# Optimization experiments

Hardware: AMD Instinct MI355X
Metric: run time of the kernel (lower is better)

## Reference

```python
import jax, jax.numpy as jnp
import numpy as np

EPS = 1e-5

def _layernorm(x, gamma, beta):
    # normalize over last (channel) axis, per point
    mu = jnp.mean(x, axis=-1, keepdims=True)
    var = jnp.mean(jnp.square(x - mu), axis=-1, keepdims=True)
    return (x - mu) * jax.lax.rsqrt(var + EPS) * gamma + beta

def setup_inputs() -> dict:
    key = jax.random.key(0)
    ks = jax.random.split(key, 12)
    B, N, C, F = 32, 4096, 3, 1024
    points = jax.random.normal(ks[0], (B, N, C), dtype=jnp.float32)
    mask = jax.random.randint(ks[1], (B, 1, N), 0, 2, dtype=jnp.int32)
    s = 0.05
    return {
        "points": points,
        "mask": mask,
        "w1": jax.random.normal(ks[2], (128, C), dtype=jnp.float32) * s,      # conv1 (no bias)
        "g1": jnp.ones((128,), jnp.float32),                                   # norm1 gamma
        "be1": jnp.zeros((128,), jnp.float32),                                 # norm1 beta
        "w2": jax.random.normal(ks[3], (256, 128), dtype=jnp.float32) * s,     # conv2
        "b2": jax.random.normal(ks[4], (256,), dtype=jnp.float32) * s,
        "w3": jax.random.normal(ks[5], (512, 512), dtype=jnp.float32) * s,     # conv3 (no bias)
        "g2": jnp.ones((512,), jnp.float32),                                   # norm2 gamma
        "be2": jnp.zeros((512,), jnp.float32),                                 # norm2 beta
        "w4": jax.random.normal(ks[6], (F, 512), dtype=jnp.float32) * s,       # conv4
        "b4": jax.random.normal(ks[7], (F,), dtype=jnp.float32) * s,
    }

def reference(points, mask, w1, g1, be1, w2, b2, w3, g2, be2, w4, b4):
    # points: [B, N, C]; mask: [B, 1, N]
    vis = (mask[:, 0, :] != 0).astype(points.dtype)[..., None]  # [B, N, 1]
    # conv1 (1x1, no bias) as point-wise matmul
    h0 = jnp.einsum('bnc,kc->bnk', points, w1)                  # [B, N, 128]
    # masked LayerNorm: LN is per-point over channels, so compute densely and zero invisible points
    h1 = _layernorm(h0, g1, be1) * vis
    h2 = jax.nn.relu(h1)
    h3 = jnp.einsum('bnk,ok->bno', h2, w2) + b2                 # [B, N, 256]
    gmax = jnp.max(h3, axis=1, keepdims=True)                   # [B, 1, 256]
    dist = jnp.concatenate([jnp.broadcast_to(gmax, h3.shape), h3], axis=-1)  # [B, N, 512]
    h4 = jnp.einsum('bno,po->bnp', dist, w3)                    # [B, N, 512]
    h5 = _layernorm(h4, g2, be2) * vis
    h6 = jax.nn.relu(h5)
    h7 = jnp.einsum('bnp,fp->bnf', h6, w4) + b4                 # [B, N, F]
    return jnp.max(h7, axis=1)                                  # [B, F]
```

## Files before the change

### kernel.cpp

```cpp
#include <hip/hip_runtime.h>
#include <stdint.h>

#define LN_EPS 1e-5f

static __device__ __forceinline__ unsigned short f2bf_bits(float f) {
  union { float f; unsigned u; } v; v.f = f;
  unsigned r = v.u + 0x7FFFu + ((v.u >> 16) & 1u);
  return (unsigned short)(r >> 16);
}
static __device__ __forceinline__ float bf2f(unsigned short h) {
  union { unsigned u; float f; } v; v.u = ((unsigned)h) << 16;
  return v.f;
}

typedef __bf16 bf16x8 __attribute__((ext_vector_type(8)));
typedef float floatx4 __attribute__((ext_vector_type(4)));

typedef __attribute__((address_space(1))) unsigned int* gas_ptr;
typedef __attribute__((address_space(3))) unsigned int* las_ptr;
static __device__ __forceinline__ void async_cp16(const void* g, void* l) {
  __builtin_amdgcn_global_load_lds((gas_ptr)g, (las_ptr)l, 16, 0, 0);
}

__global__ __launch_bounds__(256) void perm_kernel(
    const int* __restrict__ mask, int* __restrict__ newrow, int* __restrict__ cnt) {
  const int b = blockIdx.x, t = threadIdx.x;
  const int base = b * 4096 + t * 16;
  int v[16]; int s = 0;
#pragma unroll
  for (int i = 0; i < 16; ++i) { v[i] = (mask[base + i] != 0); s += v[i]; }
  const int lane = t & 63, wv = t >> 6;
  int scan = s;
  for (int o = 1; o < 64; o <<= 1) { int x = __shfl_up(scan, o); if (lane >= o) scan += x; }
  __shared__ int wsum[4], woff[4], stotal;
  if (lane == 63) wsum[wv] = scan;
  __syncthreads();
  if (t == 0) { int a = 0; for (int k = 0; k < 4; ++k) { woff[k] = a; a += wsum[k]; } stotal = a; cnt[b] = a; }
  __syncthreads();
  const int excl = scan - s + woff[wv];
  const int total = stotal;
  int run = 0;
#pragma unroll
  for (int i = 0; i < 16; ++i) {
    const int pos = t * 16 + i;
    const int visBefore = excl + run;
    newrow[b * 4096 + pos] = v[i] ? visBefore : total + (pos - visBefore);
    run += v[i];
  }
}

__global__ __launch_bounds__(256) void conv1_ln_kernel(
    const float* __restrict__ points,
    const float* __restrict__ w1, const float* __restrict__ g1,
    const float* __restrict__ be1, unsigned short* __restrict__ h2,
    const int* __restrict__ newrow, const int* __restrict__ cnt,
    const float* __restrict__ w2, const float* __restrict__ b2,
    const float* __restrict__ w3, const float* __restrict__ w4,
    unsigned short* __restrict__ w2b, unsigned short* __restrict__ w4b,
    unsigned short* __restrict__ w23b, float* __restrict__ vecb) {
  if (blockIdx.x >= 32768) {
    const int bb = blockIdx.x - 32768;
    if (bb < 2176) {
      int idx = bb * 256 + threadIdx.x;
      if (idx < 32768) w2b[idx] = f2bf_bits(w2[idx]);
      else w4b[idx - 32768] = f2bf_bits(w4[idx - 32768]);
    } else {
      const int tid = threadIdx.x;
      const int p = (bb - 2176) * 2 + (tid >> 7);
      const int c = tid & 127;
      const float* w3r = w3 + (size_t)p * 512 + 256;
      float s = 0.f;
      for (int k = 0; k < 256; ++k) s += w3r[k] * w2[k * 128 + c];
      w23b[p * 128 + c] = f2bf_bits(s);
      if (c == 0) {
        float vb = 0.f;
        for (int k = 0; k < 256; ++k) vb += w3r[k] * b2[k];
        vecb[p] = vb;
      }
    }
    return;
  }
  const int lane = threadIdx.x & 63;
  const int wv = threadIdx.x >> 6;
  const size_t p = (size_t)blockIdx.x * 4 + wv;
  const int dest = newrow[p];
  const int cntb = cnt[p >> 12];
  const int ceilv = (cntb + 127) & ~127;
  if (dest >= ceilv) return;
  const bool vis = (dest < cntb);
  const float x0 = points[p * 3 + 0];
  const float x1 = points[p * 3 + 1];
  const float x2 = points[p * 3 + 2];
  const int c0 = lane * 2, c1 = c0 + 1;
  float h00 = w1[c0 * 3] * x0 + w1[c0 * 3 + 1] * x1 + w1[c0 * 3 + 2] * x2;
  float h01 = w1[c1 * 3] * x0 + w1[c1 * 3 + 1] * x1 + w1[c1 * 3 + 2] * x2;
  float s = h00 + h01;
  for (int o = 32; o; o >>= 1) s += __shfl_xor(s, o);
  const float mu = s * (1.f / 128.f);
  const float d0 = h00 - mu, d1 = h01 - mu;
  float q = d0 * d0 + d1 * d1;
  for (int o = 32; o; o >>= 1) q += __shfl_xor(q, o);
  const float rs = rsqrtf(q * (1.f / 128.f) + LN_EPS);
  const float y0 = vis ? fmaxf(d0 * rs * g1[c0] + be1[c0], 0.f) : 0.f;
  const float y1 = vis ? fmaxf(d1 * rs * g1[c1] + be1[c1], 0.f) : 0.f;
  union { unsigned u; unsigned short s2[2]; } pk;
  pk.s2[0] = f2bf_bits(y0);
  pk.s2[1] = f2bf_bits(y1);
  const size_t prow = (p & ~(size_t)4095) + (size_t)dest;
  ((unsigned*)h2)[prow * 64 + lane] = pk.u;
}

__global__ __launch_bounds__(256) void gemm23_fused(
    const unsigned short* __restrict__ A,
    const unsigned short* __restrict__ w2b, const unsigned short* __restrict__ w23b,
    unsigned short* __restrict__ h46, float* __restrict__ pg,
    const float* __restrict__ b2, const float* __restrict__ vecb,
    const int* __restrict__ cnt, int M) {
  __shared__ __align__(16) char smA[2][128 * 64];
  __shared__ __align__(16) char smB[2][128 * 64];
  __shared__ float lmax[2][128];

  const int tid = threadIdx.x;
  const int lane = tid & 63;
  const int w = tid >> 6;
  const int wm = w >> 1, wn = w & 1;

  const int gid = blockIdx.x;
  const int xcd = gid & 7;
  const int slot = gid >> 3;
  const int rowsPerXcd = (M >> 7) >> 3;
  const int rowTile = xcd * rowsPerXcd + slot / 6;
  const int colTile = slot % 6;
  const bool isPG = (colTile < 2);
  const int colBase = isPG ? colTile * 128 : (colTile - 2) * 128;
  const size_t rowBase = (size_t)rowTile * 128;
  const unsigned short* Bw = isPG ? w2b : w23b;

  const int cntb = cnt[rowBase >> 12];
  const int rb = (int)(rowBase & 4095);
  if (rb >= cntb) {
    if (isPG) {
      if (tid < 128) pg[(size_t)rowTile * 256 + colBase + tid] = b2[colBase + tid];
    }
    return;
  }

  floatx4 acc[4][4];
  const floatx4 zero = {0.f, 0.f, 0.f, 0.f};
#pragma unroll
  for (int i = 0; i < 4; ++i)
#pragma unroll
    for (int j = 0; j < 4; ++j) acc[i][j] = zero;

  const int rSub = lane >> 2;
  const int cb16 = (lane & 3) * 16;
  const size_t Kb = 256;
  const char* gA = (const char*)A + (rowBase + (size_t)(w * 32 + rSub)) * Kb + cb16;
  const char* gB = (const char*)Bw + ((size_t)colBase + (size_t)(w * 32 + rSub)) * Kb + cb16;
  char* lA0 = smA[0] + w * 2048;
  char* lA1 = smA[1] + w * 2048;
  char* lB0 = smB[0] + w * 2048;
  char* lB1 = smB[1] + w * 2048;
  const size_t skip16 = 16 * Kb;

  const int fm = lane & 15, fq = lane >> 4;
  const int fOff = fm * 64 + fq * 16;
  const char* pa0 = smA[0] + wm * 64 * 64 + fOff;
  const char* pa1 = smA[1] + wm * 64 * 64 + fOff;
  const char* pb0 = smB[0] + wn * 64 * 64 + fOff;
  const char* pb1 = smB[1] + wn * 64 * 64 + fOff;

  for (int k0 = 0; k0 < 128; k0 += 64) {
    async_cp16(gA, lA0);
    async_cp16(gA + skip16, lA0 + 1024);
    async_cp16(gA + 64, lA1);
    async_cp16(gA + 64 + skip16, lA1 + 1024);
    async_cp16(gB, lB0);
    async_cp16(gB + skip16, lB0 + 1024);
    async_cp16(gB + 64, lB1);
    async_cp16(gB + 64 + skip16, lB1 + 1024);
    gA += 128; gB += 128;
    __syncthreads();
    bf16x8 af0[4], bg0[4], af1[4], bg1[4];
#pragma unroll
    for (int i = 0; i < 4; ++i) af0[i] = *(const bf16x8*)(pa0 + i * 16 * 64);
#pragma unroll
    for (int j = 0; j < 4; ++j) bg0[j] = *(const bf16x8*)(pb0 + j * 16 * 64);
#pragma unroll
    for (int i = 0; i < 4; ++i)
#pragma unroll
      for (int j = 0; j < 4; ++j)
        acc[i][j] = __builtin_amdgcn_mfma_f32_16x16x32_bf16(af0[i], bg0[j], acc[i][j], 0, 0, 0);
#pragma unroll
    for (int i = 0; i < 4; ++i) af1[i] = *(const bf16x8*)(pa1 + i * 16 * 64);
#pragma unroll
    for (int j = 0; j < 4; ++j) bg1[j] = *(const bf16x8*)(pb1 + j * 16 * 64);
#pragma unroll
    for (int i = 0; i < 4; ++i)
#pragma unroll
      for (int j = 0; j < 4; ++j)
        acc[i][j] = __builtin_amdgcn_mfma_f32_16x16x32_bf16(af1[i], bg1[j], acc[i][j], 0, 0, 0);
    __syncthreads();
  }

  if (isPG) {
    float m4[4] = {-1e30f, -1e30f, -1e30f, -1e30f};
#pragma unroll
    for (int j = 0; j < 4; ++j) {
      const float ex = b2[colBase + wn * 64 + j * 16 + fm];
#pragma unroll
      for (int i = 0; i < 4; ++i)
#pragma unroll
        for (int r = 0; r < 4; ++r) m4[j] = fmaxf(m4[j], acc[i][j][r] + ex);
      m4[j] = fmaxf(m4[j], __shfl_xor(m4[j], 16));
      m4[j] = fmaxf(m4[j], __shfl_xor(m4[j], 32));
    }
    const float sel = (fq == 0) ? m4[0] : (fq == 1) ? m4[1] : (fq == 2) ? m4[2] : m4[3];
    lmax[wm][wn * 64 + fq * 16 + fm] = sel;
    __syncthreads();
    if (tid < 128) {
      const float v = fmaxf(lmax[0][tid], lmax[1][tid]);
      pg[(size_t)rowTile * 256 + colBase + tid] = v;
    }
  } else {
#pragma unroll
    for (int j = 0; j < 4; ++j) {
      const int col = colBase + wn * 64 + j * 16 + fm;
      const float ex = vecb[col];
#pragma unroll
      for (int i = 0; i < 4; ++i) {
        const size_t row0 = rowBase + wm * 64 + i * 16 + fq * 4;
#pragma unroll
        for (int r = 0; r < 4; ++r) {
          h46[(row0 + r) * 512 + col] = f2bf_bits(acc[i][j][r] + ex);
        }
      }
    }
  }
}

template <int NCT>
__global__ __launch_bounds__(256) void gemm4_kernel(
    const unsigned short* __restrict__ A, const unsigned short* __restrict__ Bw,
    float* __restrict__ outp2, const int* __restrict__ cnt,
    int M, int N, int K) {
  __shared__ __align__(16) char smA[2][128 * 64];
  __shared__ __align__(16) char smB[2][128 * 64];
  __shared__ float lmax[2][128];

  const int tid = threadIdx.x;
  const int lane = tid & 63;
  const int w = tid >> 6;
  const int wm = w >> 1, wn = w & 1;

  const int gid = blockIdx.x;
  const int xcd = gid & 7;
  const int slot = gid >> 3;
  const int rowsPerXcd = (M >> 7) >> 3;
  const int rowTile = xcd * rowsPerXcd + slot / NCT;
  const int colTile = slot % NCT;
  const size_t rowBase = (size_t)rowTile * 128;
  const int colBase = colTile * 128;

  const int cntb = cnt[rowBase >> 12];
  const int rb = (int)(rowBase & 4095);
  if (rb >= cntb) {
    if (tid < 128) outp2[(size_t)rowTile * N + colBase + tid] = 0.f;
    return;
  }

  floatx4 acc[4][4];
  const floatx4 zero = {0.f, 0.f, 0.f, 0.f};
#pragma unroll
  for (int i = 0; i < 4; ++i)
#pragma unroll
    for (int j = 0; j < 4; ++j) acc[i][j] = zero;

  const int rSub = lane >> 2;
  const int cb16 = (lane & 3) * 16;
  const size_t Kb = (size_t)K * 2;
  const char* gA = (const char*)A + (rowBase + (size_t)(w * 32 + rSub)) * Kb + cb16;
  const char* gB = (const char*)Bw + ((size_t)colBase + (size_t)(w * 32 + rSub)) * Kb + cb16;
  char* lA0 = smA[0] + w * 2048;
  char* lA1 = smA[1] + w * 2048;
  char* lB0 = smB[0] + w * 2048;
  char* lB1 = smB[1] + w * 2048;
  const size_t skip16 = 16 * Kb;

  const int fm = lane & 15, fq = lane >> 4;
  const int fOff = fm * 64 + fq * 16;
  const char* pa0 = smA[0] + wm * 64 * 64 + fOff;
  const char* pa1 = smA[1] + wm * 64 * 64 + fOff;
  const char* pb0 = smB[0] + wn * 64 * 64 + fOff;
  const char* pb1 = smB[1] + wn * 64 * 64 + fOff;

  for (int k0 = 0; k0 < K; k0 += 64) {
    async_cp16(gA, lA0);
    async_cp16(gA + skip16, lA0 + 1024);
    async_cp16(gA + 64, lA1);
    async_cp16(gA + 64 + skip16, lA1 + 1024);
    async_cp16(gB, lB0);
    async_cp16(gB + skip16, lB0 + 1024);
    async_cp16(gB + 64, lB1);
    async_cp16(gB + 64 + skip16, lB1 + 1024);
    gA += 128; gB += 128;
    __syncthreads();
    bf16x8 af0[4], bg0[4], af1[4], bg1[4];
#pragma unroll
    for (int i = 0; i < 4; ++i) af0[i] = *(const bf16x8*)(pa0 + i * 16 * 64);
#pragma unroll
    for (int j = 0; j < 4; ++j) bg0[j] = *(const bf16x8*)(pb0 + j * 16 * 64);
#pragma unroll
    for (int i = 0; i < 4; ++i)
#pragma unroll
      for (int j = 0; j < 4; ++j)
        acc[i][j] = __builtin_amdgcn_mfma_f32_16x16x32_bf16(af0[i], bg0[j], acc[i][j], 0, 0, 0);
#pragma unroll
    for (int i = 0; i < 4; ++i) af1[i] = *(const bf16x8*)(pa1 + i * 16 * 64);
#pragma unroll
    for (int j = 0; j < 4; ++j) bg1[j] = *(const bf16x8*)(pb1 + j * 16 * 64);
#pragma unroll
    for (int i = 0; i < 4; ++i)
#pragma unroll
      for (int j = 0; j < 4; ++j)
        acc[i][j] = __builtin_amdgcn_mfma_f32_16x16x32_bf16(af1[i], bg1[j], acc[i][j], 0, 0, 0);
    __syncthreads();
  }

  float m4[4] = {-1e30f, -1e30f, -1e30f, -1e30f};
#pragma unroll
  for (int j = 0; j < 4; ++j) {
#pragma unroll
    for (int i = 0; i < 4; ++i)
#pragma unroll
      for (int r = 0; r < 4; ++r) m4[j] = fmaxf(m4[j], acc[i][j][r]);
    m4[j] = fmaxf(m4[j], __shfl_xor(m4[j], 16));
    m4[j] = fmaxf(m4[j], __shfl_xor(m4[j], 32));
  }
  const float sel = (fq == 0) ? m4[0] : (fq == 1) ? m4[1] : (fq == 2) ? m4[2] : m4[3];
  lmax[wm][wn * 64 + fq * 16 + fm] = sel;
  __syncthreads();
  if (tid < 128) {
    const float v = fmaxf(lmax[0][tid], lmax[1][tid]);
    outp2[(size_t)rowTile * N + colBase + tid] = v;
  }
}

__global__ __launch_bounds__(256) void gmax_cvec_kernel(
    const float* __restrict__ pg, const float* __restrict__ w3,
    float* __restrict__ cvec) {
  __shared__ float gm[256];
  const int b = blockIdx.x >> 2, quarter = blockIdx.x & 3;
  const int t = threadIdx.x;
  float m = -1e30f;
  for (int s = 0; s < 32; ++s) m = fmaxf(m, pg[((size_t)b * 32 + s) * 256 + t]);
  gm[t] = m;
  __syncthreads();
  const int lane = t & 63, wv = t >> 6;
  const float g0 = gm[lane * 4 + 0];
  const float g1 = gm[lane * 4 + 1];
  const float g2v = gm[lane * 4 + 2];
  const float g3 = gm[lane * 4 + 3];
  for (int pp = 0; pp < 32; ++pp) {
    const int p = quarter * 128 + wv * 32 + pp;
    const float4 wr = *(const float4*)(w3 + (size_t)p * 512 + lane * 4);
    float s = wr.x * g0 + wr.y * g1 + wr.z * g2v + wr.w * g3;
    for (int o = 32; o; o >>= 1) s += __shfl_xor(s, o);
    if (lane == 0) cvec[b * 512 + p] = s;
  }
}

__global__ __launch_bounds__(256) void ln2_kernel(
    unsigned short* __restrict__ h46, const int* __restrict__ cnt,
    const float* __restrict__ cvec,
    const float* __restrict__ g2, const float* __restrict__ be2) {
  const int lane = threadIdx.x & 63;
  const int wv = threadIdx.x >> 6;
  const size_t p = (size_t)blockIdx.x * 4 + wv;
  const int cb = cnt[p >> 12];
  const int pin = (int)(p & 4095);
  const int ceilv = (cb + 127) & ~127;
  if (pin >= ceilv) return;
  unsigned short* row = h46 + p * 512;
  const int c0 = lane * 8;
  if (pin >= cb) {
    const uint4 z = {0, 0, 0, 0};
    *(uint4*)(row + c0) = z;
    return;
  }
  const int b = (int)(p >> 12);
  union { uint4 v; unsigned short s[8]; } in;
  in.v = *(const uint4*)(row + c0);
  float cv[8];
  *(float4*)(cv) = *(const float4*)(cvec + b * 512 + c0);
  *(float4*)(cv + 4) = *(const float4*)(cvec + b * 512 + c0 + 4);
  float f[8];
  float s = 0.f;
#pragma unroll
  for (int k = 0; k < 8; ++k) { f[k] = bf2f(in.s[k]) + cv[k]; s += f[k]; }
  for (int o = 32; o; o >>= 1) s += __shfl_xor(s, o);
  const float mu = s * (1.f / 512.f);
  float q = 0.f;
#pragma unroll
  for (int k = 0; k < 8; ++k) { const float d = f[k] - mu; q += d * d; }
  for (int o = 32; o; o >>= 1) q += __shfl_xor(q, o);
  const float rs = rsqrtf(q * (1.f / 512.f) + LN_EPS);
  union { uint4 v; unsigned short s[8]; } outv;
#pragma unroll
  for (int k = 0; k < 8; ++k) {
    const float y = fmaxf((f[k] - mu) * rs * g2[c0 + k] + be2[c0 + k], 0.f);
    outv.s[k] = f2bf_bits(y);
  }
  *(uint4*)(row + c0) = outv.v;
}

__global__ __launch_bounds__(256) void final_kernel(
    const float* __restrict__ pmax, const float* __restrict__ b4,
    float* __restrict__ out) {
  const int idx = blockIdx.x * 256 + threadIdx.x;
  const int b = idx >> 10, f = idx & 1023;
  float m = -1e30f;
  for (int r = 0; r < 32; ++r) m = fmaxf(m, pmax[((size_t)(b * 32 + r)) * 1024 + f]);
  out[idx] = m + b4[f];
}

extern "C" void kernel_launch(void* const* d_in, const int* in_sizes, int n_in,
                              void* d_out, int out_size, void* d_ws, size_t ws_size,
                              hipStream_t stream) {
  const float* points = (const float*)d_in[0];
  const int* mask = (const int*)d_in[1];
  const float* w1 = (const float*)d_in[2];
  const float* g1 = (const float*)d_in[3];
  const float* be1 = (const float*)d_in[4];
  const float* w2 = (const float*)d_in[5];
  const float* b2 = (const float*)d_in[6];
  const float* w3 = (const float*)d_in[7];
  const float* g2 = (const float*)d_in[8];
  const float* be2 = (const float*)d_in[9];
  const float* w4 = (const float*)d_in[10];
  const float* b4 = (const float*)d_in[11];
  float* out = (float*)d_out;
  char* ws = (char*)d_ws;

  const size_t OFF_H46 = 0;
  const size_t OFF_H2 = 134217728;
  const size_t OFF_W2B = OFF_H2 + 33554432;
  const size_t OFF_W4B = OFF_W2B + 65536;
  const size_t OFF_W23B = OFF_W4B + 1048576;
  const size_t OFF_VECB = OFF_W23B + 131072;
  const size_t OFF_PG = OFF_VECB + 2048;
  const size_t OFF_CVEC = OFF_PG + 1048576;
  const size_t OFF_PMAX = OFF_CVEC + 65536;
  const size_t OFF_CNT = OFF_PMAX + 4194304;
  const size_t OFF_NEWROW = OFF_CNT + 4096;

  unsigned short* h2 = (unsigned short*)(ws + OFF_H2);
  unsigned short* h46 = (unsigned short*)(ws + OFF_H46);
  unsigned short* w2b = (unsigned short*)(ws + OFF_W2B);
  unsigned short* w4b = (unsigned short*)(ws + OFF_W4B);
  unsigned short* w23b = (unsigned short*)(ws + OFF_W23B);
  float* vecb = (float*)(ws + OFF_VECB);
  float* pg = (float*)(ws + OFF_PG);
  float* cvecp = (float*)(ws + OFF_CVEC);
  float* pmaxp = (float*)(ws + OFF_PMAX);
  int* cntp = (int*)(ws + OFF_CNT);
  int* newrow = (int*)(ws + OFF_NEWROW);

  perm_kernel<<<32, 256, 0, stream>>>(mask, newrow, cntp);
  conv1_ln_kernel<<<32768 + 2176 + 256, 256, 0, stream>>>(
      points, w1, g1, be1, h2, newrow, cntp, w2, b2, w3, w4, w2b, w4b, w23b, vecb);
  gemm23_fused<<<6144, 256, 0, stream>>>(h2, w2b, w23b, h46, pg, b2, vecb, cntp, 131072);
  gmax_cvec_kernel<<<128, 256, 0, stream>>>(pg, w3, cvecp);
  ln2_kernel<<<32768, 256, 0, stream>>>(h46, cntp, cvecp, g2, be2);
  gemm4_kernel<8><<<8192, 256, 0, stream>>>(h46, w4b, pmaxp, cntp, 131072, 1024, 512);
  final_kernel<<<128, 256, 0, stream>>>(pmaxp, b4, out);
}
```

Baseline: 278.8 us.

## Rewrite final GEMM as 256x256-tile 8-phase pipelined kernel with swizzled LDS

Replaces the 128x128, 4-wave gemm4 kernel with a 256x256-tile, 8-wave kernel using 128KB dynamic LDS. It double-buffers K-slices through explicit vmcnt/lgkmcnt waits, barriers and setprio, and uses an XOR-swizzled LDS layout to avoid bank conflicts. The aim is to raise arithmetic intensity per load and overlap global-to-LDS copies with MFMA work. Coarser 256-row tiles mean more padded rows are computed and zero-filled, so ln2 and final_kernel are adjusted to match.

```diff
diff --git a/kernel.cpp b/kernel.cpp
--- a/kernel.cpp
+++ b/kernel.cpp
@@ -239,110 +239,152 @@
   }
 }
 
-template <int NCT>
-__global__ __launch_bounds__(256) void gemm4_kernel(
+#define G4_BAR() __builtin_amdgcn_s_barrier()
+#define G4_LGKM0() asm volatile("s_waitcnt lgkmcnt(0)" ::: "memory")
+#define G4_LGKM8() asm volatile("s_waitcnt lgkmcnt(8)" ::: "memory")
+#define G4_VM2() asm volatile("s_waitcnt vmcnt(2)" ::: "memory")
+#define G4_VM0() asm volatile("s_waitcnt vmcnt(0)" ::: "memory")
+#define G4_PRIO1() __builtin_amdgcn_s_setprio(1)
+#define G4_PRIO0() __builtin_amdgcn_s_setprio(0)
+
+#define G4_STG(bufi, h4, kt) do { \
+  const char* _s = (((h4) < 2) ? srcA : srcB) + (size_t)((h4) & 1) * (128 * 1024) + (size_t)(kt) * 128; \
+  char* _d = stDst + (bufi) * 65536 + ((h4) >> 1) * 32768 + ((h4) & 1) * 16384; \
+  async_cp16(_s, _d); \
+  async_cp16(_s + 64 * 1024, _d + 8192); \
+} while (0)
+
+#define G4_LDA(bufi, mh) do { \
+  const char* _p = rdA + (bufi) * 65536 + (mh) * 8192; \
+  af[0][0] = *(const bf16x8*)(_p + c0);        af[0][1] = *(const bf16x8*)(_p + c1); \
+  af[1][0] = *(const bf16x8*)(_p + 2048 + c0); af[1][1] = *(const bf16x8*)(_p + 2048 + c1); \
+  af[2][0] = *(const bf16x8*)(_p + 4096 + c0); af[2][1] = *(const bf16x8*)(_p + 4096 + c1); \
+  af[3][0] = *(const bf16x8*)(_p + 6144 + c0); af[3][1] = *(const bf16x8*)(_p + 6144 + c1); \
+} while (0)
+
+#define G4_LDB(bufi, nh, bgx) do { \
+  const char* _p = rdB + (bufi) * 65536 + (nh) * 4096; \
+  bgx[0][0] = *(const bf16x8*)(_p + c0);        bgx[0][1] = *(const bf16x8*)(_p + c1); \
+  bgx[1][0] = *(const bf16x8*)(_p + 2048 + c0); bgx[1][1] = *(const bf16x8*)(_p + 2048 + c1); \
+} while (0)
+
+#define G4_QUAD(mh, nh, bgx) do { \
+  _Pragma("unroll") \
+  for (int _m = 0; _m < 4; ++_m) { \
+    _Pragma("unroll") \
+    for (int _n = 0; _n < 2; ++_n) { \
+      acc[(mh) * 4 + _m][(nh) * 2 + _n] = __builtin_amdgcn_mfma_f32_16x16x32_bf16( \
+          af[_m][0], bgx[_n][0], acc[(mh) * 4 + _m][(nh) * 2 + _n], 0, 0, 0); \
+      acc[(mh) * 4 + _m][(nh) * 2 + _n] = __builtin_amdgcn_mfma_f32_16x16x32_bf16( \
+          af[_m][1], bgx[_n][1], acc[(mh) * 4 + _m][(nh) * 2 + _n], 0, 0, 0); \
+    } \
+  } \
+} while (0)
+
+__global__ __launch_bounds__(512, 2) void gemm4_8ph(
     const unsigned short* __restrict__ A, const unsigned short* __restrict__ Bw,
-    float* __restrict__ outp2, const int* __restrict__ cnt,
-    int M, int N, int K) {
-  __shared__ __align__(16) char smA[2][128 * 64];
-  __shared__ __align__(16) char smB[2][128 * 64];
-  __shared__ float lmax[2][128];
+    float* __restrict__ outp2, const int* __restrict__ cnt) {
+  extern __shared__ char sm[];
 
   const int tid = threadIdx.x;
   const int lane = tid & 63;
   const int w = tid >> 6;
-  const int wm = w >> 1, wn = w & 1;
+  const int wm = w >> 2, wn = w & 3;
 
   const int gid = blockIdx.x;
   const int xcd = gid & 7;
   const int slot = gid >> 3;
-  const int rowsPerXcd = (M >> 7) >> 3;
-  const int rowTile = xcd * rowsPerXcd + slot / NCT;
-  const int colTile = slot % NCT;
-  const size_t rowBase = (size_t)rowTile * 128;
-  const int colBase = colTile * 128;
+  const int rowTile = xcd * 64 + (slot >> 2);
+  const int colTile = slot & 3;
+  const size_t rowBase = (size_t)rowTile * 256;
+  const int colBase = colTile * 256;
 
   const int cntb = cnt[rowBase >> 12];
   const int rb = (int)(rowBase & 4095);
   if (rb >= cntb) {
-    if (tid < 128) outp2[(size_t)rowTile * N + colBase + tid] = 0.f;
+    if (tid < 256) outp2[(size_t)rowTile * 1024 + colBase + tid] = 0.f;
     return;
   }
 
-  floatx4 acc[4][4];
+  const int rr = tid >> 3;
+  const int csw = ((tid & 7) ^ (rr & 7)) << 4;
+  const char* srcA = (const char*)A + (rowBase + (size_t)rr) * 1024 + csw;
+  const char* srcB = (const char*)Bw + ((size_t)colBase + (size_t)rr) * 1024 + csw;
+  char* stDst = sm + w * 1024;
+
+  const int fr = lane & 15, fq = lane >> 4;
+  const int c0 = (fq * 16) ^ ((lane & 7) << 4);
+  const int c1 = ((fq * 16) | 64) ^ ((lane & 7) << 4);
+  const char* rdA = sm + (wm * 128 + fr) * 128;
+  const char* rdB = sm + 32768 + (wn * 64 + fr) * 128;
+
+  floatx4 acc[8][4];
   const floatx4 zero = {0.f, 0.f, 0.f, 0.f};
 #pragma unroll
-  for (int i = 0; i < 4; ++i)
+  for (int i = 0; i < 8; ++i)
 #pragma unroll
     for (int j = 0; j < 4; ++j) acc[i][j] = zero;
 
-  const int rSub = lane >> 2;
-  const int cb16 = (lane & 3) * 16;
-  const size_t Kb = (size_t)K * 2;
-  const char* gA = (const char*)A + (rowBase + (size_t)(w * 32 + rSub)) * Kb + cb16;
-  const char* gB = (const char*)Bw + ((size_t)colBase + (size_t)(w * 32 + rSub)) * Kb + cb16;
-  char* lA0 = smA[0] + w * 2048;
-  char* lA1 = smA[1] + w * 2048;
-  char* lB0 = smB[0] + w * 2048;
-  char* lB1 = smB[1] + w * 2048;
-  const size_t skip16 = 16 * Kb;
-
-  const int fm = lane & 15, fq = lane >> 4;
-  const int fOff = fm * 64 + fq * 16;
-  const char* pa0 = smA[0] + wm * 64 * 64 + fOff;
-  const char* pa1 = smA[1] + wm * 64 * 64 + fOff;
-  const char* pb0 = smB[0] + wn * 64 * 64 + fOff;
-  const char* pb1 = smB[1] + wn * 64 * 64 + fOff;
-
-  for (int k0 = 0; k0 < K; k0 += 64) {
-    async_cp16(gA, lA0);
-    async_cp16(gA + skip16, lA0 + 1024);
-    async_cp16(gA + 64, lA1);
-    async_cp16(gA + 64 + skip16, lA1 + 1024);
-    async_cp16(gB, lB0);
-    async_cp16(gB + skip16, lB0 + 1024);
-    async_cp16(gB + 64, lB1);
-    async_cp16(gB + 64 + skip16, lB1 + 1024);
-    gA += 128; gB += 128;
-    __syncthreads();
-    bf16x8 af0[4], bg0[4], af1[4], bg1[4];
-#pragma unroll
-    for (int i = 0; i < 4; ++i) af0[i] = *(const bf16x8*)(pa0 + i * 16 * 64);
-#pragma unroll
-    for (int j = 0; j < 4; ++j) bg0[j] = *(const bf16x8*)(pb0 + j * 16 * 64);
-#pragma unroll
-    for (int i = 0; i < 4; ++i)
-#pragma unroll
-      for (int j = 0; j < 4; ++j)
-        acc[i][j] = __builtin_amdgcn_mfma_f32_16x16x32_bf16(af0[i], bg0[j], acc[i][j], 0, 0, 0);
-#pragma unroll
-    for (int i = 0; i < 4; ++i) af1[i] = *(const bf16x8*)(pa1 + i * 16 * 64);
-#pragma unroll
-    for (int j = 0; j < 4; ++j) bg1[j] = *(const bf16x8*)(pb1 + j * 16 * 64);
-#pragma unroll
-    for (int i = 0; i < 4; ++i)
-#pragma unroll
-      for (int j = 0; j < 4; ++j)
-        acc[i][j] = __builtin_amdgcn_mfma_f32_16x16x32_bf16(af1[i], bg1[j], acc[i][j], 0, 0, 0);
-    __syncthreads();
-  }
-
-  float m4[4] = {-1e30f, -1e30f, -1e30f, -1e30f};
-#pragma unroll
-  for (int j = 0; j < 4; ++j) {
-#pragma unroll
-    for (int i = 0; i < 4; ++i)
-#pragma unroll
-      for (int r = 0; r < 4; ++r) m4[j] = fmaxf(m4[j], acc[i][j][r]);
-    m4[j] = fmaxf(m4[j], __shfl_xor(m4[j], 16));
-    m4[j] = fmaxf(m4[j], __shfl_xor(m4[j], 32));
-  }
-  const float sel = (fq == 0) ? m4[0] : (fq == 1) ? m4[1] : (fq == 2) ? m4[2] : m4[3];
-  lmax[wm][wn * 64 + fq * 16 + fm] = sel;
+  bf16x8 af[4][2], bg0[2][2], bg1[2][2];
+
+  G4_STG(0, 0, 0); G4_STG(0, 1, 0); G4_STG(0, 2, 0); G4_STG(0, 3, 0);
+  G4_STG(1, 0, 1);
+  G4_VM2(); G4_BAR();
+
+  for (int it = 0; it < 3; ++it) {
+    const int tO = 2 * it + 1, tE2 = 2 * it + 2, tO2 = 2 * it + 3;
+    G4_LDA(0, 0); G4_LDB(0, 0, bg0); G4_STG(1, 1, tO); G4_LGKM8(); G4_BAR(); G4_LGKM0();
+    G4_PRIO1(); G4_QUAD(0, 0, bg0); G4_PRIO0(); G4_BAR();
+    G4_LDB(0, 1, bg1); G4_STG(1, 2, tO); G4_BAR(); G4_LGKM0();
+    G4_PRIO1(); G4_QUAD(0, 1, bg1); G4_PRIO0(); G4_BAR();
+    G4_LDA(0, 1); G4_STG(1, 3, tO); G4_BAR(); G4_LGKM0();
+    G4_PRIO1(); G4_QUAD(1, 1, bg1); G4_PRIO0(); G4_BAR();
+    G4_STG(0, 0, tE2); G4_VM2(); G4_BAR();
+    G4_PRIO1(); G4_QUAD(1, 0, bg0); G4_PRIO0(); G4_BAR();
+    G4_LDA(1, 0); G4_LDB(1, 0, bg0); G4_STG(0, 1, tE2); G4_LGKM8(); G4_BAR(); G4_LGKM0();
+    G4_PRIO1(); G4_QUAD(0, 0, bg0); G4_PRIO0(); G4_BAR();
+    G4_LDB(1, 1, bg1); G4_STG(0, 2, tE2); G4_BAR(); G4_LGKM0();
+    G4_PRIO1(); G4_QUAD(0, 1, bg1); G4_PRIO0(); G4_BAR();
+    G4_LDA(1, 1); G4_STG(0, 3, tE2); G4_BAR(); G4_LGKM0();
+    G4_PRIO1(); G4_QUAD(1, 1, bg1); G4_PRIO0(); G4_BAR();
+    G4_STG(1, 0, tO2); G4_VM2(); G4_BAR();
+    G4_PRIO1(); G4_QUAD(1, 0, bg0); G4_PRIO0(); G4_BAR();
+  }
+
+  G4_LDA(0, 0); G4_LDB(0, 0, bg0); G4_STG(1, 1, 7); G4_LGKM8(); G4_BAR(); G4_LGKM0();
+  G4_PRIO1(); G4_QUAD(0, 0, bg0); G4_PRIO0(); G4_BAR();
+  G4_LDB(0, 1, bg1); G4_STG(1, 2, 7); G4_BAR(); G4_LGKM0();
+  G4_PRIO1(); G4_QUAD(0, 1, bg1); G4_PRIO0(); G4_BAR();
+  G4_LDA(0, 1); G4_STG(1, 3, 7); G4_BAR(); G4_LGKM0();
+  G4_PRIO1(); G4_QUAD(1, 1, bg1); G4_PRIO0(); G4_BAR();
+  G4_VM0(); G4_BAR();
+  G4_PRIO1(); G4_QUAD(1, 0, bg0); G4_PRIO0(); G4_BAR();
+  G4_LDA(1, 0); G4_LDB(1, 0, bg0); G4_BAR(); G4_LGKM0();
+  G4_PRIO1(); G4_QUAD(0, 0, bg0); G4_PRIO0(); G4_BAR();
+  G4_LDB(1, 1, bg1); G4_BAR(); G4_LGKM0();
+  G4_PRIO1(); G4_QUAD(0, 1, bg1); G4_PRIO0(); G4_BAR();
+  G4_LDA(1, 1); G4_BAR(); G4_LGKM0();
+  G4_PRIO1(); G4_QUAD(1, 1, bg1); G4_PRIO0(); G4_BAR();
+  G4_PRIO1(); G4_QUAD(1, 0, bg0); G4_PRIO0(); G4_BAR();
+
+  float* smf = (float*)sm;
+  float mv[4];
+#pragma unroll
+  for (int nj = 0; nj < 4; ++nj) {
+    float m = -1e30f;
+#pragma unroll
+    for (int mi = 0; mi < 8; ++mi)
+#pragma unroll
+      for (int r = 0; r < 4; ++r) m = fmaxf(m, acc[mi][nj][r]);
+    m = fmaxf(m, __shfl_xor(m, 16));
+    m = fmaxf(m, __shfl_xor(m, 32));
+    mv[nj] = m;
+  }
+  const float sel = (fq == 0) ? mv[0] : (fq == 1) ? mv[1] : (fq == 2) ? mv[2] : mv[3];
+  smf[wm * 256 + wn * 64 + fq * 16 + fr] = sel;
   __syncthreads();
-  if (tid < 128) {
-    const float v = fmaxf(lmax[0][tid], lmax[1][tid]);
-    outp2[(size_t)rowTile * N + colBase + tid] = v;
+  if (tid < 256) {
+    outp2[(size_t)rowTile * 1024 + colBase + tid] = fmaxf(smf[tid], smf[256 + tid]);
   }
 }
 
@@ -379,7 +421,7 @@
   const size_t p = (size_t)blockIdx.x * 4 + wv;
   const int cb = cnt[p >> 12];
   const int pin = (int)(p & 4095);
-  const int ceilv = (cb + 127) & ~127;
+  const int ceilv = (cb + 255) & ~255;
   if (pin >= ceilv) return;
   unsigned short* row = h46 + p * 512;
   const int c0 = lane * 8;
@@ -420,7 +462,7 @@
   const int idx = blockIdx.x * 256 + threadIdx.x;
   const int b = idx >> 10, f = idx & 1023;
   float m = -1e30f;
-  for (int r = 0; r < 32; ++r) m = fmaxf(m, pmax[((size_t)(b * 32 + r)) * 1024 + f]);
+  for (int r = 0; r < 16; ++r) m = fmaxf(m, pmax[((size_t)(b * 16 + r)) * 1024 + f]);
   out[idx] = m + b4[f];
 }
 
@@ -466,12 +508,19 @@
   int* cntp = (int*)(ws + OFF_CNT);
   int* newrow = (int*)(ws + OFF_NEWROW);
 
+  static bool s_attr_done = false;
+  if (!s_attr_done) {
+    hipFuncSetAttribute((const void*)gemm4_8ph,
+                        hipFuncAttributeMaxDynamicSharedMemorySize, 131072);
+    s_attr_done = true;
+  }
+
   perm_kernel<<<32, 256, 0, stream>>>(mask, newrow, cntp);
   conv1_ln_kernel<<<32768 + 2176 + 256, 256, 0, stream>>>(
       points, w1, g1, be1, h2, newrow, cntp, w2, b2, w3, w4, w2b, w4b, w23b, vecb);
   gemm23_fused<<<6144, 256, 0, stream>>>(h2, w2b, w23b, h46, pg, b2, vecb, cntp, 131072);
   gmax_cvec_kernel<<<128, 256, 0, stream>>>(pg, w3, cvecp);
   ln2_kernel<<<32768, 256, 0, stream>>>(h46, cntp, cvecp, g2, be2);
-  gemm4_kernel<8><<<8192, 256, 0, stream>>>(h46, w4b, pmaxp, cntp, 131072, 1024, 512);
+  gemm4_8ph<<<2048, 512, 131072, stream>>>(h46, w4b, pmaxp, cntp);
   final_kernel<<<128, 256, 0, stream>>>(pmaxp, b4, out);
 }
```

Measured after the change: 268.1 us. -3.8%, faster.
